# Kernel optimization log

Hardware: AMD Instinct MI355X
Metric: run time of the kernel (lower is better)

The kernel has to match this reference:

```python
import jax, jax.numpy as jnp
import numpy as np

B, N, E = 64, 4096, 32768
F_IN, H = 12, 64
K1 = int(np.ceil(0.8 * N))    # TopKPooling ratio=0.8 -> 3277
K2 = int(np.ceil(0.8 * K1))   # -> 2622


def _lin(key, o, i):
    s = 1.0 / np.sqrt(i)
    return jax.random.uniform(key, (o, i), jnp.float32, -s, s)


def setup_inputs() -> dict:
    key = jax.random.key(0)
    ks = jax.random.split(key, 16)
    return {
        "x": jax.random.normal(ks[0], (B, N, F_IN), jnp.float32),
        "edge_index": jax.random.randint(ks[1], (B, 2, E), 0, N),
        # GraphConv 1: lin_rel (with bias) on aggregated msgs, lin_root (no bias)
        "W1_rel": _lin(ks[2], H, F_IN),
        "b1": jnp.zeros((H,), jnp.float32),
        "W1_root": _lin(ks[3], H, F_IN),
        # TopKPooling 1 projection vector
        "p1": jax.random.normal(ks[4], (H,), jnp.float32),
        # GraphConv 2
        "W2_rel": _lin(ks[5], H, H),
        "b2": jnp.zeros((H,), jnp.float32),
        "W2_root": _lin(ks[6], H, H),
        "p2": jax.random.normal(ks[7], (H,), jnp.float32),
        # heads
        "Wa1": _lin(ks[8], 64, 128),
        "ba1": jnp.zeros((64,), jnp.float32),
        "Wa5": _lin(ks[9], 10, 64),
        "ba5": jnp.zeros((10,), jnp.float32),
    }


def _graph_conv(x, src, dst, emask, Wr, br, Wn, n):
    # PyG GraphConv: lin_rel(sum_{j->i} x_j) + lin_root(x_i); masked edges send 0
    msg = x[src] * emask[:, None]                      # [E, d]
    agg = jax.ops.segment_sum(msg, dst, num_segments=n)  # [n, d]
    return agg @ Wr.T + br + x @ Wn.T


def _topk_pool(x, src, dst, emask, p, k):
    # score = x.p/||p||; keep top-k nodes, gate by tanh(score); mask dropped edges
    n = x.shape[0]
    score = (x @ p) / jnp.linalg.norm(p)
    vals, perm = jax.lax.top_k(score, k)
    xk = x[perm] * jnp.tanh(vals)[:, None]
    pos = jnp.full((n,), -1, jnp.int32).at[perm].set(jnp.arange(k, dtype=jnp.int32))
    ns, nd = pos[src], pos[dst]
    valid = (ns >= 0) & (nd >= 0) & (emask > 0)
    return xk, jnp.where(valid, ns, 0), jnp.where(valid, nd, 0), valid.astype(x.dtype)


def reference(x, edge_index, W1_rel, b1, W1_root, p1, W2_rel, b2, W2_root, p2, Wa1, ba1, Wa5, ba5):
    def per_graph(xg, eig):
        src, dst = eig[0], eig[1]
        emask = jnp.ones((src.shape[0],), xg.dtype)
        h = jax.nn.relu(_graph_conv(xg, src, dst, emask, W1_rel, b1, W1_root, N))
        h, src, dst, emask = _topk_pool(h, src, dst, emask, p1, K1)
        x1 = jnp.concatenate([h.max(axis=0), h.mean(axis=0)])   # gmp || gap -> [128]
        h = jax.nn.relu(_graph_conv(h, src, dst, emask, W2_rel, b2, W2_root, K1))
        h, src, dst, emask = _topk_pool(h, src, dst, emask, p2, K2)
        x2 = jnp.concatenate([h.max(axis=0), h.mean(axis=0)])
        return x1 + x2

    feats = jax.vmap(per_graph)(x, edge_index)                  # [B, 128]
    a1 = jax.nn.relu(feats @ Wa1.T + ba1)
    a5 = a1 @ Wa5.T + ba5                                       # [B, 10]
    # F.softmax(dim=0).unsqueeze(0): softmax ACROSS graphs, then add leading dim
    return jax.nn.softmax(a5, axis=0)[None]                     # [1, B, 10]
```

## Files before the change

### kernel.cpp

```cpp
#include <hip/hip_runtime.h>
#include <float.h>
#include <math.h>

#define BB 64
#define NN 4096
#define EE 32768
#define FIN 12
#define HD 64
#define KK1 3277
#define KK2 2622
#define TB1 52
#define RB2 16

__global__ __launch_bounds__(1024) void k_csr(const int* __restrict__ ei,
    int* __restrict__ row_ofs, int* __restrict__ esrc, int g0) {
  __shared__ int cnt[NN];
  __shared__ int part[1024];
  int s = blockIdx.x, g = g0 + s, t = threadIdx.x;
  const int* src = ei + (size_t)g * 2 * EE;
  const int* dst = src + EE;
  for (int i = t; i < NN; i += 1024) cnt[i] = 0;
  __syncthreads();
  for (int e = t; e < EE; e += 1024) atomicAdd(&cnt[dst[e]], 1);
  __syncthreads();
  int c0 = cnt[t * 4], c1 = cnt[t * 4 + 1], c2 = cnt[t * 4 + 2], c3 = cnt[t * 4 + 3];
  int tot = c0 + c1 + c2 + c3;
  part[t] = tot;
  __syncthreads();
  for (int off = 1; off < 1024; off <<= 1) {
    int v = part[t];
    int add = (t >= off) ? part[t - off] : 0;
    __syncthreads();
    part[t] = v + add;
    __syncthreads();
  }
  int base = part[t] - tot;
  int b0 = base, b1 = base + c0, b2 = b1 + c1, b3 = b2 + c2;
  cnt[t * 4] = b0; cnt[t * 4 + 1] = b1; cnt[t * 4 + 2] = b2; cnt[t * 4 + 3] = b3;
  int* RO = row_ofs + (size_t)s * (NN + 1);
  RO[t * 4] = b0; RO[t * 4 + 1] = b1; RO[t * 4 + 2] = b2; RO[t * 4 + 3] = b3;
  if (t == 0) RO[NN] = EE;
  __syncthreads();
  int* ES = esrc + (size_t)s * EE;
  for (int e = t; e < EE; e += 1024) {
    int p = atomicAdd(&cnt[dst[e]], 1);
    ES[p] = src[e];
  }
}

__global__ __launch_bounds__(256, 4) void k_h1f(const float* __restrict__ x,
    const int* __restrict__ row_ofs, const int* __restrict__ esrc,
    const float* __restrict__ W1r, const float* __restrict__ b1,
    const float* __restrict__ W1n, const float* __restrict__ p1,
    float* __restrict__ h1, float* __restrict__ score1, int g0, int G8) {
  __shared__ float sWr[64 * FIN], sWn[64 * FIN], sb[64], sp[64];
  __shared__ float sCol[32][257];
  int tid = threadIdx.x;
  for (int i = tid; i < 64 * FIN; i += 256) {
    sWr[i] = W1r[i];
    sWn[i] = W1n[i];
  }
  if (tid < 64) { sb[tid] = b1[tid]; sp[tid] = p1[tid]; }
  __syncthreads();
  int b = blockIdx.x, s, nb;
  if (G8 > 0) { int hi = b >> 3; s = (b & 7) * G8 + hi / 16; nb = hi % 16; }
  else { s = b >> 4; nb = b & 15; }
  int node = nb * 256 + tid;
  int g = g0 + s;
  float nq = 0.f;
#pragma unroll
  for (int k = 0; k < 64; k++) nq += sp[k] * sp[k];
  float inv_norm = 1.0f / sqrtf(nq);
  const int* RO = row_ofs + (size_t)s * (NN + 1);
  const int* ES = esrc + (size_t)s * EE;
  const float4* X4 = (const float4*)(x + (size_t)g * NN * FIN);
  int r0 = RO[node], r1 = RO[node + 1];
  float a[FIN];
#pragma unroll
  for (int f = 0; f < FIN; f++) a[f] = 0.f;
  for (int i = r0; i < r1; i++) {
    int so = ES[i];
    float4 v0 = X4[(size_t)so * 3];
    float4 v1 = X4[(size_t)so * 3 + 1];
    float4 v2 = X4[(size_t)so * 3 + 2];
    a[0] += v0.x; a[1] += v0.y; a[2]  += v0.z; a[3]  += v0.w;
    a[4] += v1.x; a[5] += v1.y; a[6]  += v1.z; a[7]  += v1.w;
    a[8] += v2.x; a[9] += v2.y; a[10] += v2.z; a[11] += v2.w;
  }
  float xr[FIN];
  {
    float4 u0 = X4[(size_t)node * 3];
    float4 u1 = X4[(size_t)node * 3 + 1];
    float4 u2 = X4[(size_t)node * 3 + 2];
    xr[0] = u0.x; xr[1] = u0.y; xr[2]  = u0.z; xr[3]  = u0.w;
    xr[4] = u1.x; xr[5] = u1.y; xr[6]  = u1.z; xr[7]  = u1.w;
    xr[8] = u2.x; xr[9] = u2.y; xr[10] = u2.z; xr[11] = u2.w;
  }
  float* hbase = h1 + ((size_t)s * NN + (size_t)nb * 256) * HD;
  float v = 0.f;
  for (int half = 0; half < 2; half++) {
#pragma unroll
    for (int k0 = 0; k0 < 32; k0++) {
      int k = half * 32 + k0;
      const float* wr = &sWr[k * FIN];
      const float* wn = &sWn[k * FIN];
      float acc = sb[k];
#pragma unroll
      for (int f = 0; f < FIN; f++) acc += a[f] * wr[f] + xr[f] * wn[f];
      acc = fmaxf(acc, 0.f);
      v += acc * sp[k];
      sCol[k0][tid] = acc;
    }
    __syncthreads();
    float* hb = hbase + half * 32;
    for (int i = tid; i < 256 * 32; i += 256) {
      int nd = i >> 5, c = i & 31;
      hb[(size_t)nd * HD + c] = sCol[c][nd];
    }
    __syncthreads();
  }
  score1[(size_t)s * NN + node] = v * inv_norm;
}

__global__ __launch_bounds__(1024) void k_select(const float* __restrict__ score,
    int scStride, int nvalid, int K, int* __restrict__ sel, int selStride,
    int* __restrict__ pos, int posStride, float* __restrict__ tgo) {
  __shared__ unsigned int keys[4096];
  __shared__ int hist[257];
  __shared__ int part[1024];
  __shared__ unsigned int sh_pref;
  __shared__ int sh_rem;
  int s = blockIdx.x, t = threadIdx.x;
  const float* sc = score + (size_t)s * scStride;
  for (int i = t; i < 4096; i += 1024) {
    unsigned int key = 0u;
    if (i < nvalid) {
      unsigned int bb = __float_as_uint(sc[i]);
      key = (bb & 0x80000000u) ? ~bb : (bb | 0x80000000u);
    }
    keys[i] = key;
  }
  if (t == 0) { sh_pref = 0u; sh_rem = K; }
  __syncthreads();
  for (int sh = 24; sh >= 0; sh -= 8) {
    unsigned int pref = sh_pref;
    int rem = sh_rem;
    if (t < 256) hist[t] = 0;
    __syncthreads();
    for (int i = t; i < 4096; i += 1024) {
      unsigned int u = keys[i];
      bool in = (sh == 24) || ((u >> (sh + 8)) == pref);
      if (in) atomicAdd(&hist[(u >> sh) & 255], 1);
    }
    __syncthreads();
    for (int off = 1; off < 256; off <<= 1) {
      int v = 0;
      if (t < 256) { v = hist[t]; if (t + off < 256) v += hist[t + off]; }
      __syncthreads();
      if (t < 256) hist[t] = v;
      __syncthreads();
    }
    if (t < 256) {
      int ge = hist[t];
      int gt_ = (t == 255) ? 0 : hist[t + 1];
      if (ge >= rem && gt_ < rem) {
        sh_pref = (pref << 8) | (unsigned int)t;
        sh_rem = rem - gt_;
      }
    }
    __syncthreads();
  }
  unsigned int thr = sh_pref;
  int remEq = sh_rem;
  uint4 kk = *(const uint4*)&keys[4 * t];
  int eq0 = (kk.x == thr), eq1 = (kk.y == thr), eq2 = (kk.z == thr), eq3 = (kk.w == thr);
  int eqc = eq0 + eq1 + eq2 + eq3;
  part[t] = eqc;
  __syncthreads();
  for (int off = 1; off < 1024; off <<= 1) {
    int v = part[t];
    int add = (t >= off) ? part[t - off] : 0;
    __syncthreads();
    part[t] = v + add;
    __syncthreads();
  }
  int e_run = part[t] - eqc;
  int kp0 = (kk.x > thr) || (eq0 && (e_run < remEq)); e_run += eq0;
  int kp1 = (kk.y > thr) || (eq1 && (e_run < remEq)); e_run += eq1;
  int kp2 = (kk.z > thr) || (eq2 && (e_run < remEq)); e_run += eq2;
  int kp3 = (kk.w > thr) || (eq3 && (e_run < remEq));
  int kc = kp0 + kp1 + kp2 + kp3;
  __syncthreads();
  part[t] = kc;
  __syncthreads();
  for (int off = 1; off < 1024; off <<= 1) {
    int v = part[t];
    int add = (t >= off) ? part[t - off] : 0;
    __syncthreads();
    part[t] = v + add;
    __syncthreads();
  }
  int r = part[t] - kc;
  int kp[4] = {kp0, kp1, kp2, kp3};
#pragma unroll
  for (int q = 0; q < 4; q++) {
    int i = 4 * t + q;
    if (i < nvalid) {
      if (kp[q]) {
        if (sel) sel[(size_t)s * selStride + r] = i;
        if (pos) pos[(size_t)s * posStride + i] = r;
        if (tgo) tgo[(size_t)s * NN + i] = tanhf(sc[i]);
      } else {
        if (pos) pos[(size_t)s * posStride + i] = -1;
        if (tgo) tgo[(size_t)s * NN + i] = 0.f;
      }
    }
    r += kp[q];
  }
}

__global__ __launch_bounds__(256) void k_fuse(const float* __restrict__ h1,
    const int* __restrict__ row_ofs, const int* __restrict__ esrc,
    const int* __restrict__ sel1, const float* __restrict__ tgo,
    const float* __restrict__ W2r, const float* __restrict__ W2n,
    const float* __restrict__ b2, const float* __restrict__ p2,
    float* __restrict__ h2, float* __restrict__ score2,
    float* __restrict__ pmax, float* __restrict__ psum, int G8) {
  __shared__ float sWT[128 * 64];
  __shared__ float sG[64 * 132];
  __shared__ float redm[4][64], reds[4][64];
  int b = blockIdx.x, s, tb;
  if (G8 > 0) { int hi = b >> 3; s = (b & 7) * G8 + hi / TB1; tb = hi % TB1; }
  else { s = b / TB1; tb = b % TB1; }
  int tid = threadIdx.x;
  int j0 = tb * 64;
  int nv = KK1 - j0; if (nv > 64) nv = 64;
  for (int i = tid; i < 128 * 64; i += 256) {
    int k = i >> 6, c = i & 63;
    sWT[i] = (k < 64) ? W2r[c * 64 + k] : W2n[c * 64 + (k - 64)];
  }
  {
    int r = tid >> 2, q = tid & 3;
    float4 a0 = {0.f,0.f,0.f,0.f}, a1 = a0, a2 = a0, a3 = a0;
    float4 s0 = a0, s1 = a0, s2 = a0, s3 = a0;
    if (r < nv) {
      int j = j0 + r;
      int d = sel1[(size_t)s * KK1 + j];
      const int* RO = row_ofs + (size_t)s * (NN + 1);
      const int* ES = esrc + (size_t)s * EE;
      const float* H = h1 + (size_t)s * NN * HD;
      const float* TG = tgo + (size_t)s * NN;
      const float4* hd = (const float4*)(H + (size_t)d * HD + q * 16);
      float td = TG[d];
      s0 = hd[0]; s1 = hd[1]; s2 = hd[2]; s3 = hd[3];
      s0.x *= td; s0.y *= td; s0.z *= td; s0.w *= td;
      s1.x *= td; s1.y *= td; s1.z *= td; s1.w *= td;
      s2.x *= td; s2.y *= td; s2.z *= td; s2.w *= td;
      s3.x *= td; s3.y *= td; s3.z *= td; s3.w *= td;
      int e0 = RO[d], e1 = RO[d + 1];
      for (int e = e0; e < e1; e++) {
        int o = ES[e];
        float w = TG[o];
        const float4* ho = (const float4*)(H + (size_t)o * HD + q * 16);
        float4 v0 = ho[0], v1 = ho[1], v2 = ho[2], v3 = ho[3];
        a0.x += w * v0.x; a0.y += w * v0.y; a0.z += w * v0.z; a0.w += w * v0.w;
        a1.x += w * v1.x; a1.y += w * v1.y; a1.z += w * v1.z; a1.w += w * v1.w;
        a2.x += w * v2.x; a2.y += w * v2.y; a2.z += w * v2.z; a2.w += w * v2.w;
        a3.x += w * v3.x; a3.y += w * v3.y; a3.z += w * v3.z; a3.w += w * v3.w;
      }
    }
    float* gw = &sG[r * 132 + q * 16];
    ((float4*)gw)[0] = a0; ((float4*)gw)[1] = a1;
    ((float4*)gw)[2] = a2; ((float4*)gw)[3] = a3;
    float* gs = &sG[r * 132 + 64 + q * 16];
    ((float4*)gs)[0] = s0; ((float4*)gs)[1] = s1;
    ((float4*)gs)[2] = s2; ((float4*)gs)[3] = s3;
  }
  __syncthreads();
  {
    int c = tid & 63, qq = tid >> 6;
    float mx = -FLT_MAX, sm = 0.f;
    int rend = qq * 16 + 16; if (rend > nv) rend = nv;
    for (int rr = qq * 16; rr < rend; rr++) {
      float v = sG[rr * 132 + 64 + c];
      mx = fmaxf(mx, v); sm += v;
    }
    redm[qq][c] = mx; reds[qq][c] = sm;
  }
  __syncthreads();
  if (tid < 64) {
    float mx = redm[0][tid], sm = reds[0][tid];
    for (int qq = 1; qq < 4; qq++) { mx = fmaxf(mx, redm[qq][tid]); sm += reds[qq][tid]; }
    pmax[((size_t)s * TB1 + tb) * 64 + tid] = mx;
    psum[((size_t)s * TB1 + tb) * 64 + tid] = sm;
  }
  int rb = (tid >> 4) * 4;
  int c0 = (tid & 15) * 4;
  float acc[4][4];
#pragma unroll
  for (int i = 0; i < 4; i++)
#pragma unroll
    for (int cc = 0; cc < 4; cc++) acc[i][cc] = 0.f;
  for (int k = 0; k < 128; k += 4) {
    float4 w0 = *(const float4*)&sWT[(k + 0) * 64 + c0];
    float4 w1 = *(const float4*)&sWT[(k + 1) * 64 + c0];
    float4 w2 = *(const float4*)&sWT[(k + 2) * 64 + c0];
    float4 w3 = *(const float4*)&sWT[(k + 3) * 64 + c0];
#pragma unroll
    for (int i = 0; i < 4; i++) {
      float4 g = *(const float4*)&sG[(rb + i) * 132 + k];
      acc[i][0] += g.x * w0.x + g.y * w1.x + g.z * w2.x + g.w * w3.x;
      acc[i][1] += g.x * w0.y + g.y * w1.y + g.z * w2.y + g.w * w3.y;
      acc[i][2] += g.x * w0.z + g.y * w1.z + g.z * w2.z + g.w * w3.z;
      acc[i][3] += g.x * w0.w + g.y * w1.w + g.z * w2.w + g.w * w3.w;
    }
  }
  float4 b2v = *(const float4*)&b2[c0];
  float4 p2v = *(const float4*)&p2[c0];
  float nq = p2v.x * p2v.x + p2v.y * p2v.y + p2v.z * p2v.z + p2v.w * p2v.w;
  nq += __shfl_xor(nq, 1, 64);
  nq += __shfl_xor(nq, 2, 64);
  nq += __shfl_xor(nq, 4, 64);
  nq += __shfl_xor(nq, 8, 64);
  float inv_norm = 1.0f / sqrtf(nq);
  float vs[4];
#pragma unroll
  for (int i = 0; i < 4; i++) {
    int j = j0 + rb + i;
    float4 h;
    h.x = fmaxf(acc[i][0] + b2v.x, 0.f);
    h.y = fmaxf(acc[i][1] + b2v.y, 0.f);
    h.z = fmaxf(acc[i][2] + b2v.z, 0.f);
    h.w = fmaxf(acc[i][3] + b2v.w, 0.f);
    if (j < KK1) *(float4*)&h2[((size_t)s * KK1 + j) * 64 + c0] = h;
    vs[i] = h.x * p2v.x + h.y * p2v.y + h.z * p2v.z + h.w * p2v.w;
  }
#pragma unroll
  for (int i = 0; i < 4; i++) {
    vs[i] += __shfl_xor(vs[i], 1, 64);
    vs[i] += __shfl_xor(vs[i], 2, 64);
    vs[i] += __shfl_xor(vs[i], 4, 64);
    vs[i] += __shfl_xor(vs[i], 8, 64);
  }
  if ((tid & 15) == 0) {
#pragma unroll
    for (int i = 0; i < 4; i++) {
      int j = j0 + rb + i;
      if (j < KK1) score2[(size_t)s * KK1 + j] = vs[i] * inv_norm;
    }
  }
}

__global__ __launch_bounds__(64) void k_read1r(const float* __restrict__ pmax,
    const float* __restrict__ psum, float* __restrict__ x1) {
  int s = blockIdx.x, k = threadIdx.x;
  float mx = -FLT_MAX, sm = 0.f;
  for (int t = 0; t < TB1; t++) {
    mx = fmaxf(mx, pmax[((size_t)s * TB1 + t) * 64 + k]);
    sm += psum[((size_t)s * TB1 + t) * 64 + k];
  }
  x1[(size_t)s * 128 + k] = mx;
  x1[(size_t)s * 128 + 64 + k] = sm / (float)KK1;
}

__global__ __launch_bounds__(256) void k_read2p(const float* __restrict__ h2,
    const int* __restrict__ pos2, const float* __restrict__ score2,
    float* __restrict__ p2max, float* __restrict__ p2sum) {
  int s = blockIdx.x / RB2, pb = blockIdx.x % RB2;
  int lane = threadIdx.x & 63, wave = threadIdx.x >> 6;
  const int ROWS = (KK1 + RB2 - 1) / RB2;
  int j0 = pb * ROWS;
  int j1 = j0 + ROWS; if (j1 > KK1) j1 = KK1;
  float mx = -FLT_MAX, sm = 0.f;
  for (int j = j0 + wave; j < j1; j += 4) {
    if (pos2[(size_t)s * KK1 + j] >= 0) {
      float t = tanhf(score2[(size_t)s * KK1 + j]);
      float v = h2[((size_t)s * KK1 + j) * HD + lane] * t;
      mx = fmaxf(mx, v); sm += v;
    }
  }
  __shared__ float smx[4][64], ssm[4][64];
  smx[wave][lane] = mx; ssm[wave][lane] = sm;
  __syncthreads();
  if (wave == 0) {
    for (int q = 1; q < 4; q++) { mx = fmaxf(mx, smx[q][lane]); sm += ssm[q][lane]; }
    p2max[((size_t)s * RB2 + pb) * 64 + lane] = mx;
    p2sum[((size_t)s * RB2 + pb) * 64 + lane] = sm;
  }
}

__global__ __launch_bounds__(64) void k_read2r(const float* __restrict__ p2max,
    const float* __restrict__ p2sum, const float* __restrict__ x1,
    float* __restrict__ feats, int g0) {
  int s = blockIdx.x, k = threadIdx.x;
  float mx = -FLT_MAX, sm = 0.f;
  for (int t = 0; t < RB2; t++) {
    mx = fmaxf(mx, p2max[((size_t)s * RB2 + t) * 64 + k]);
    sm += p2sum[((size_t)s * RB2 + t) * 64 + k];
  }
  feats[(size_t)(g0 + s) * 128 + k] = x1[(size_t)s * 128 + k] + mx;
  feats[(size_t)(g0 + s) * 128 + 64 + k] = x1[(size_t)s * 128 + 64 + k] + sm / (float)KK2;
}

__global__ __launch_bounds__(256) void k_heada(const float* __restrict__ feats,
    const float* __restrict__ Wa1, const float* __restrict__ ba1,
    const float* __restrict__ Wa5, const float* __restrict__ ba5,
    float* __restrict__ a5) {
  __shared__ float sF[128];
  __shared__ float sA1[64];
  int b = blockIdx.x, t = threadIdx.x;
  if (t < 32) ((float4*)sF)[t] = ((const float4*)(feats + (size_t)b * 128))[t];
  __syncthreads();
  {
    int j = t >> 2, q = t & 3;
    const float4* w = (const float4*)(Wa1 + (size_t)j * 128 + q * 32);
    const float4* f4 = (const float4*)(sF + q * 32);
    float acc = 0.f;
#pragma unroll
    for (int i = 0; i < 8; i++) {
      float4 wv = w[i], fv = f4[i];
      acc += wv.x * fv.x + wv.y * fv.y + wv.z * fv.z + wv.w * fv.w;
    }
    acc += __shfl_xor(acc, 1, 64);
    acc += __shfl_xor(acc, 2, 64);
    if (q == 0) sA1[j] = fmaxf(acc + ba1[j], 0.f);
  }
  __syncthreads();
  if (t < 160) {
    int c = t >> 4, l = t & 15;
    float acc = 0.f;
#pragma unroll
    for (int i = 0; i < 4; i++) {
      int jj = l * 4 + i;
      acc += sA1[jj] * Wa5[c * 64 + jj];
    }
    acc += __shfl_xor(acc, 1, 64);
    acc += __shfl_xor(acc, 2, 64);
    acc += __shfl_xor(acc, 4, 64);
    acc += __shfl_xor(acc, 8, 64);
    if (l == 0) a5[b * 10 + c] = acc + ba5[c];
  }
}

__global__ __launch_bounds__(64) void k_headb(const float* __restrict__ a5,
    float* __restrict__ out) {
  int c = threadIdx.x;
  if (c < 10) {
    float m = -FLT_MAX;
    for (int b = 0; b < BB; b++) m = fmaxf(m, a5[b * 10 + c]);
    float sum = 0.f;
    for (int b = 0; b < BB; b++) sum += expf(a5[b * 10 + c] - m);
    float inv = 1.0f / sum;
    for (int b = 0; b < BB; b++) out[b * 10 + c] = expf(a5[b * 10 + c] - m) * inv;
  }
}

extern "C" void kernel_launch(void* const* d_in, const int* in_sizes, int n_in,
                              void* d_out, int out_size, void* d_ws, size_t ws_size,
                              hipStream_t stream) {
  const float* x   = (const float*)d_in[0];
  const int*   ei  = (const int*)d_in[1];
  const float* W1r = (const float*)d_in[2];
  const float* b1  = (const float*)d_in[3];
  const float* W1n = (const float*)d_in[4];
  const float* p1  = (const float*)d_in[5];
  const float* W2r = (const float*)d_in[6];
  const float* b2  = (const float*)d_in[7];
  const float* W2n = (const float*)d_in[8];
  const float* p2  = (const float*)d_in[9];
  const float* Wa1 = (const float*)d_in[10];
  const float* ba1 = (const float*)d_in[11];
  const float* Wa5 = (const float*)d_in[12];
  const float* ba5 = (const float*)d_in[13];
  float* out = (float*)d_out;

  char* base = (char*)d_ws;
  size_t off = 0;
  auto alloc = [&](size_t bytes) -> void* {
    void* p = base + off;
    off = (off + bytes + 255) & ~(size_t)255;
    return p;
  };
  float* feats = (float*)alloc((size_t)BB * 128 * 4);
  float* a5buf = (float*)alloc((size_t)BB * 10 * 4);

  const size_t perSlot =
      ((size_t)(NN + 1) + EE + (size_t)NN * HD + NN + KK1 + NN +
       (size_t)KK1 * HD + 2 * (size_t)KK1 +
       2 * (size_t)TB1 * 64 + 2 * (size_t)RB2 * 64 + 128) * 4
      + 24 * 256;
  size_t avail = ws_size > off ? ws_size - off : 0;
  int CH = (int)(avail / perSlot);
  if (CH > BB) CH = BB;
  if (CH < 1) CH = 1;

  int*   row_ofs = (int*)alloc((size_t)CH * (NN + 1) * 4);
  int*   esrc    = (int*)alloc((size_t)CH * EE * 4);
  float* h1      = (float*)alloc((size_t)CH * NN * HD * 4);
  float* score1  = (float*)alloc((size_t)CH * NN * 4);
  int*   sel1    = (int*)alloc((size_t)CH * KK1 * 4);
  float* tgo     = (float*)alloc((size_t)CH * NN * 4);
  float* h2      = (float*)alloc((size_t)CH * KK1 * HD * 4);
  float* score2  = (float*)alloc((size_t)CH * KK1 * 4);
  int*   pos2    = (int*)alloc((size_t)CH * KK1 * 4);
  float* pmax    = (float*)alloc((size_t)CH * TB1 * 64 * 4);
  float* psum    = (float*)alloc((size_t)CH * TB1 * 64 * 4);
  float* p2max   = (float*)alloc((size_t)CH * RB2 * 64 * 4);
  float* p2sum   = (float*)alloc((size_t)CH * RB2 * 64 * 4);
  float* x1      = (float*)alloc((size_t)CH * 128 * 4);

  for (int g0 = 0; g0 < BB; g0 += CH) {
    int G = (BB - g0) < CH ? (BB - g0) : CH;
    int G8 = (G % 8 == 0) ? G / 8 : 0;
    k_csr<<<G, 1024, 0, stream>>>(ei, row_ofs, esrc, g0);
    k_h1f<<<G * 16, 256, 0, stream>>>(x, row_ofs, esrc, W1r, b1, W1n, p1, h1, score1, g0, G8);
    k_select<<<G, 1024, 0, stream>>>(score1, NN, NN, KK1, sel1, KK1, nullptr, 0, tgo);
    k_fuse<<<G * TB1, 256, 0, stream>>>(h1, row_ofs, esrc, sel1, tgo, W2r, W2n, b2, p2,
                                        h2, score2, pmax, psum, G8);
    k_select<<<G, 1024, 0, stream>>>(score2, KK1, KK1, KK2, nullptr, 0, pos2, KK1, nullptr);
    k_read1r<<<G, 64, 0, stream>>>(pmax, psum, x1);
    k_read2p<<<G * RB2, 256, 0, stream>>>(h2, pos2, score2, p2max, p2sum);
    k_read2r<<<G, 64, 0, stream>>>(p2max, p2sum, x1, feats, g0);
  }
  k_heada<<<BB, 256, 0, stream>>>(feats, Wa1, ba1, Wa5, ba5, a5buf);
  k_headb<<<1, 64, 0, stream>>>(a5buf, out);
}
```

Measured before the change: 343.1 us.

## Drop shared weight staging in k_fuse, unroll edge gather, overlap reduction with matmul

Removes the 32 KB shared-memory transposed weight tile in k_fuse and reads W2_rel/W2_root rows straight from global (L1/L2-cached) inside the small matmul. The launch-bounds hint is raised to 4 blocks per CU. The CSR neighbour gather is unrolled by two with a second accumulator set to put more loads in flight. The max/sum partial reduction now runs before a barrier that the matmul work sits in front of, so the two can overlap. The cost is more register pressure and global weight loads that are uncoalesced across lanes.

```diff
diff --git a/kernel.cpp b/kernel.cpp
--- a/kernel.cpp
+++ b/kernel.cpp
@@ -219,14 +219,13 @@
   }
 }
 
-__global__ __launch_bounds__(256) void k_fuse(const float* __restrict__ h1,
+__global__ __launch_bounds__(256, 4) void k_fuse(const float* __restrict__ h1,
     const int* __restrict__ row_ofs, const int* __restrict__ esrc,
     const int* __restrict__ sel1, const float* __restrict__ tgo,
     const float* __restrict__ W2r, const float* __restrict__ W2n,
     const float* __restrict__ b2, const float* __restrict__ p2,
     float* __restrict__ h2, float* __restrict__ score2,
     float* __restrict__ pmax, float* __restrict__ psum, int G8) {
-  __shared__ float sWT[128 * 64];
   __shared__ float sG[64 * 132];
   __shared__ float redm[4][64], reds[4][64];
   int b = blockIdx.x, s, tb;
@@ -235,30 +234,48 @@
   int tid = threadIdx.x;
   int j0 = tb * 64;
   int nv = KK1 - j0; if (nv > 64) nv = 64;
-  for (int i = tid; i < 128 * 64; i += 256) {
-    int k = i >> 6, c = i & 63;
-    sWT[i] = (k < 64) ? W2r[c * 64 + k] : W2n[c * 64 + (k - 64)];
+  int r = tid >> 2, q = tid & 3;
+  bool rv = r < nv;
+  int d = 0;
+  const float* H = h1 + (size_t)s * NN * HD;
+  const float* TG = tgo + (size_t)s * NN;
+  float td = 0.f;
+  if (rv) {
+    d = sel1[(size_t)s * KK1 + j0 + r];
+    td = TG[d];
   }
   {
-    int r = tid >> 2, q = tid & 3;
     float4 a0 = {0.f,0.f,0.f,0.f}, a1 = a0, a2 = a0, a3 = a0;
+    float4 c0v = a0, c1v = a0, c2v = a0, c3v = a0;
     float4 s0 = a0, s1 = a0, s2 = a0, s3 = a0;
-    if (r < nv) {
-      int j = j0 + r;
-      int d = sel1[(size_t)s * KK1 + j];
-      const int* RO = row_ofs + (size_t)s * (NN + 1);
-      const int* ES = esrc + (size_t)s * EE;
-      const float* H = h1 + (size_t)s * NN * HD;
-      const float* TG = tgo + (size_t)s * NN;
+    if (rv) {
       const float4* hd = (const float4*)(H + (size_t)d * HD + q * 16);
-      float td = TG[d];
       s0 = hd[0]; s1 = hd[1]; s2 = hd[2]; s3 = hd[3];
       s0.x *= td; s0.y *= td; s0.z *= td; s0.w *= td;
       s1.x *= td; s1.y *= td; s1.z *= td; s1.w *= td;
       s2.x *= td; s2.y *= td; s2.z *= td; s2.w *= td;
       s3.x *= td; s3.y *= td; s3.z *= td; s3.w *= td;
+      const int* RO = row_ofs + (size_t)s * (NN + 1);
+      const int* ES = esrc + (size_t)s * EE;
       int e0 = RO[d], e1 = RO[d + 1];
-      for (int e = e0; e < e1; e++) {
+      int e = e0;
+      for (; e + 2 <= e1; e += 2) {
+        int oA = ES[e], oB = ES[e + 1];
+        float wA = TG[oA], wB = TG[oB];
+        const float4* hA = (const float4*)(H + (size_t)oA * HD + q * 16);
+        const float4* hB = (const float4*)(H + (size_t)oB * HD + q * 16);
+        float4 vA0 = hA[0], vA1 = hA[1], vA2 = hA[2], vA3 = hA[3];
+        float4 vB0 = hB[0], vB1 = hB[1], vB2 = hB[2], vB3 = hB[3];
+        a0.x += wA * vA0.x; a0.y += wA * vA0.y; a0.z += wA * vA0.z; a0.w += wA * vA0.w;
+        a1.x += wA * vA1.x; a1.y += wA * vA1.y; a1.z += wA * vA1.z; a1.w += wA * vA1.w;
+        a2.x += wA * vA2.x; a2.y += wA * vA2.y; a2.z += wA * vA2.z; a2.w += wA * vA2.w;
+        a3.x += wA * vA3.x; a3.y += wA * vA3.y; a3.z += wA * vA3.z; a3.w += wA * vA3.w;
+        c0v.x += wB * vB0.x; c0v.y += wB * vB0.y; c0v.z += wB * vB0.z; c0v.w += wB * vB0.w;
+        c1v.x += wB * vB1.x; c1v.y += wB * vB1.y; c1v.z += wB * vB1.z; c1v.w += wB * vB1.w;
+        c2v.x += wB * vB2.x; c2v.y += wB * vB2.y; c2v.z += wB * vB2.z; c2v.w += wB * vB2.w;
+        c3v.x += wB * vB3.x; c3v.y += wB * vB3.y; c3v.z += wB * vB3.z; c3v.w += wB * vB3.w;
+      }
+      if (e < e1) {
         int o = ES[e];
         float w = TG[o];
         const float4* ho = (const float4*)(H + (size_t)o * HD + q * 16);
@@ -268,6 +285,10 @@
         a2.x += w * v2.x; a2.y += w * v2.y; a2.z += w * v2.z; a2.w += w * v2.w;
         a3.x += w * v3.x; a3.y += w * v3.y; a3.z += w * v3.z; a3.w += w * v3.w;
       }
+      a0.x += c0v.x; a0.y += c0v.y; a0.z += c0v.z; a0.w += c0v.w;
+      a1.x += c1v.x; a1.y += c1v.y; a1.z += c1v.z; a1.w += c1v.w;
+      a2.x += c2v.x; a2.y += c2v.y; a2.z += c2v.z; a2.w += c2v.w;
+      a3.x += c3v.x; a3.y += c3v.y; a3.z += c3v.z; a3.w += c3v.w;
     }
     float* gw = &sG[r * 132 + q * 16];
     ((float4*)gw)[0] = a0; ((float4*)gw)[1] = a1;
@@ -287,33 +308,51 @@
     }
     redm[qq][c] = mx; reds[qq][c] = sm;
   }
+  int rb = (tid >> 4) * 4;
+  int c0 = (tid & 15) * 4;
+  float acc[4][4];
+#pragma unroll
+  for (int i = 0; i < 4; i++)
+#pragma unroll
+    for (int cc = 0; cc < 4; cc++) acc[i][cc] = 0.f;
+  const float* Wr0 = W2r + (size_t)c0 * 64;
+  const float* Wn0 = W2n + (size_t)c0 * 64;
+#pragma unroll 2
+  for (int k0 = 0; k0 < 64; k0 += 4) {
+    float4 w0 = *(const float4*)&Wr0[0 * 64 + k0];
+    float4 w1 = *(const float4*)&Wr0[1 * 64 + k0];
+    float4 w2 = *(const float4*)&Wr0[2 * 64 + k0];
+    float4 w3 = *(const float4*)&Wr0[3 * 64 + k0];
+#pragma unroll
+    for (int i = 0; i < 4; i++) {
+      float4 g = *(const float4*)&sG[(rb + i) * 132 + k0];
+      acc[i][0] += g.x * w0.x + g.y * w0.y + g.z * w0.z + g.w * w0.w;
+      acc[i][1] += g.x * w1.x + g.y * w1.y + g.z * w1.z + g.w * w1.w;
+      acc[i][2] += g.x * w2.x + g.y * w2.y + g.z * w2.z + g.w * w2.w;
+      acc[i][3] += g.x * w3.x + g.y * w3.y + g.z * w3.z + g.w * w3.w;
+    }
+  }
+#pragma unroll 2
+  for (int k0 = 0; k0 < 64; k0 += 4) {
+    float4 w0 = *(const float4*)&Wn0[0 * 64 + k0];
+    float4 w1 = *(const float4*)&Wn0[1 * 64 + k0];
+    float4 w2 = *(const float4*)&Wn0[2 * 64 + k0];
+    float4 w3 = *(const float4*)&Wn0[3 * 64 + k0];
+#pragma unroll
+    for (int i = 0; i < 4; i++) {
+      float4 g = *(const float4*)&sG[(rb + i) * 132 + 64 + k0];
+      acc[i][0] += g.x * w0.x + g.y * w0.y + g.z * w0.z + g.w * w0.w;
+      acc[i][1] += g.x * w1.x + g.y * w1.y + g.z * w1.z + g.w * w1.w;
+      acc[i][2] += g.x * w2.x + g.y * w2.y + g.z * w2.z + g.w * w2.w;
+      acc[i][3] += g.x * w3.x + g.y * w3.y + g.z * w3.z + g.w * w3.w;
+    }
+  }
   __syncthreads();
   if (tid < 64) {
     float mx = redm[0][tid], sm = reds[0][tid];
     for (int qq = 1; qq < 4; qq++) { mx = fmaxf(mx, redm[qq][tid]); sm += reds[qq][tid]; }
     pmax[((size_t)s * TB1 + tb) * 64 + tid] = mx;
     psum[((size_t)s * TB1 + tb) * 64 + tid] = sm;
-  }
-  int rb = (tid >> 4) * 4;
-  int c0 = (tid & 15) * 4;
-  float acc[4][4];
-#pragma unroll
-  for (int i = 0; i < 4; i++)
-#pragma unroll
-    for (int cc = 0; cc < 4; cc++) acc[i][cc] = 0.f;
-  for (int k = 0; k < 128; k += 4) {
-    float4 w0 = *(const float4*)&sWT[(k + 0) * 64 + c0];
-    float4 w1 = *(const float4*)&sWT[(k + 1) * 64 + c0];
-    float4 w2 = *(const float4*)&sWT[(k + 2) * 64 + c0];
-    float4 w3 = *(const float4*)&sWT[(k + 3) * 64 + c0];
-#pragma unroll
-    for (int i = 0; i < 4; i++) {
-      float4 g = *(const float4*)&sG[(rb + i) * 132 + k];
-      acc[i][0] += g.x * w0.x + g.y * w1.x + g.z * w2.x + g.w * w3.x;
-      acc[i][1] += g.x * w0.y + g.y * w1.y + g.z * w2.y + g.w * w3.y;
-      acc[i][2] += g.x * w0.z + g.y * w1.z + g.z * w2.z + g.w * w3.z;
-      acc[i][3] += g.x * w0.w + g.y * w1.w + g.z * w2.w + g.w * w3.w;
-    }
   }
   float4 b2v = *(const float4*)&b2[c0];
   float4 p2v = *(const float4*)&p2[c0];
```

Result: slower. 441.2 us (+28.6%).
